# Kernel optimization log

Hardware: AMD Instinct MI355X
Metric: run time of the kernel (lower is better)

## Reference

```python
import jax, jax.numpy as jnp
import numpy as np

N = 100000   # nodes
E = 1600000  # edges
F_IN = 64    # n_features
H = 32       # hidden_size
OUT = 1      # output_size


def _lin(k, fan_in, fan_out):
    return (jax.random.normal(k, (fan_in, fan_out), jnp.float32) / np.sqrt(fan_in)).astype(jnp.float32)


def setup_inputs() -> dict:
    key = jax.random.key(0)
    ks = jax.random.split(key, 16)
    x = jax.random.normal(ks[0], (N, F_IN), jnp.float32)
    edge_index = jax.random.randint(ks[1], (2, E), 0, N, dtype=jnp.int64)
    # guarantee current_node (=0) has outgoing edges so the legal-move mask is non-empty
    edge_index = edge_index.at[0, :64].set(0)
    edge_attr = jax.random.uniform(ks[2], (E,), jnp.float32)
    return {
        "x": x, "edge_index": edge_index, "edge_attr": edge_attr, "current_node": 0,
        # conv_in: GraphConv(F_IN -> H)
        "Win_rel": _lin(ks[3], F_IN, H), "bin_rel": jnp.zeros((H,), jnp.float32), "Win_root": _lin(ks[4], F_IN, H),
        # conv_hidden: GraphConv(H -> H)
        "Wh_rel": _lin(ks[5], H, H), "bh_rel": jnp.zeros((H,), jnp.float32), "Wh_root": _lin(ks[6], H, H),
        # policy_conv: GraphConv(H -> OUT)
        "Wp_rel": _lin(ks[7], H, OUT), "bp_rel": jnp.zeros((OUT,), jnp.float32), "Wp_root": _lin(ks[8], H, OUT),
        # value_conv: GraphConv(H -> OUT)
        "Wv_rel": _lin(ks[9], H, OUT), "bv_rel": jnp.zeros((OUT,), jnp.float32), "Wv_root": _lin(ks[10], H, OUT),
    }


def _graph_conv(h, src, dst, ew, W_rel, b_rel, W_root):
    # PyG GraphConv: out_i = W_root h_i + W_rel * sum_{j->i} e_ji * h_j + b
    msg = h[src] * ew[:, None]                              # [E, d] gather + scale
    agg = jax.ops.segment_sum(msg, dst, num_segments=N)      # [N, d] scatter-add
    return agg @ W_rel + b_rel + h @ W_root


def reference(x, edge_index, edge_attr, current_node,
              Win_rel, bin_rel, Win_root,
              Wh_rel, bh_rel, Wh_root,
              Wp_rel, bp_rel, Wp_root,
              Wv_rel, bv_rel, Wv_root):
    src, dst = edge_index[0], edge_index[1]
    h = jax.nn.relu(_graph_conv(x, src, dst, edge_attr, Win_rel, bin_rel, Win_root))
    h = jax.nn.relu(_graph_conv(h, src, dst, edge_attr, Wh_rel, bh_rel, Wh_root))
    p = _graph_conv(h, src, dst, edge_attr, Wp_rel, bp_rel, Wp_root)  # [N, 1]
    v = _graph_conv(h, src, dst, edge_attr, Wv_rel, bv_rel, Wv_root)  # [N, 1]
    # illegal_moves_mask: 1 for nodes directly reachable from current_node
    hit = (src == current_node).astype(jnp.float32)
    mask = (jnp.zeros((N,), jnp.float32).at[dst].add(hit) > 0).astype(jnp.float32)
    p_m = mask * p.T                                   # [1, N]
    p_m = jnp.where(p_m == 0, -jnp.inf, p_m)
    p_soft = jax.nn.softmax(p_m, axis=1)
    v_m = mask * v.T                                   # [1, N]
    return p_soft.reshape(-1), v_m.reshape(-1)
```

## Files before the change

### kernel.cpp

```cpp
#include <hip/hip_runtime.h>
#include <hip/hip_fp16.h>
#include <cmath>

static constexpr int NN = 100000;
static constexpr int NE = 1600000;
static const size_t NW = (size_t)NN * 32;
static constexpr int SUB = 256;
static constexpr int NSUB = 391;
static constexpr int CH = 8192;
static constexpr int NCH = (NE + CH - 1) / CH;
static constexpr int BCAP = 5200;
static constexpr int CSRN = NSUB * BCAP;
static constexpr int MCAP = 4096;

__device__ __forceinline__ float ent_w(unsigned e)
{
    return __half2float(__ushort_as_half((unsigned short)(e >> 17)));
}
__device__ __forceinline__ int ent_s(unsigned e)
{
    int s = (int)(e & 0x1FFFF);
    return s < NN ? s : NN - 1;
}

__device__ __forceinline__ float4 pack8(const float* v)
{
    union { __half2 h2[4]; float4 f4; } u;
    u.h2[0] = __floats2half2_rn(v[0], v[1]);
    u.h2[1] = __floats2half2_rn(v[2], v[3]);
    u.h2[2] = __floats2half2_rn(v[4], v[5]);
    u.h2[3] = __floats2half2_rn(v[6], v[7]);
    return u.f4;
}

__global__ void __launch_bounds__(512) fused_build_mm1_k(
    const int* __restrict__ src, const int* __restrict__ dst,
    const float* __restrict__ ew, const int* __restrict__ curp,
    int* __restrict__ maskb, int* __restrict__ mcount, int* __restrict__ mlist,
    int* __restrict__ bcnt, unsigned* __restrict__ bx,
    unsigned char* __restrict__ bd,
    const float* __restrict__ x, const float* __restrict__ Wrel,
    const float* __restrict__ Wroot, const float* __restrict__ bin,
    __half* __restrict__ proj1, __half* __restrict__ root1)
{
    __shared__ union {
        struct {
            unsigned sBufX[CH];
            unsigned char sBufD[CH];
            int lhist[NSUB];
            int lpos[NSUB];
            int lstart[NSUB];
            int lbase[NSUB];
            int tscan[512];
        } s;
        struct {
            float sX[128 * 65];
            float sW[64 * 68];
        } m;
    } u;

    int t = threadIdx.x;
    int bid = blockIdx.x;

    if (bid < NCH) {
        for (int i = t; i < NSUB; i += 512) { u.s.lhist[i] = 0; u.s.lpos[i] = 0; }
        __syncthreads();
        int c0 = bid * CH;
        int cur = curp[0];
        unsigned rx[CH / 512];
        int rd[CH / 512];
#pragma unroll
        for (int it = 0; it < CH / 512; ++it) {
            int e = c0 + it * 512 + t;
            rd[it] = -1;
            if (e < NE) {
                int d = dst[e];
                int sv = src[e];
                if ((unsigned)d < (unsigned)NN) {
                    rd[it] = d;
                    unsigned bits = __half_as_ushort(__float2half(ew[e]));
                    rx[it] = ((unsigned)sv & 0x1FFFF) | (bits << 17);
                    atomicAdd(&u.s.lhist[d >> 8], 1);
                    if (sv == cur) {
                        if (atomicExch(maskb + d, 1) == 0) {
                            int idx = atomicAdd(mcount, 1);
                            if (idx < MCAP) mlist[idx] = d;
                        }
                    }
                }
            }
        }
        __syncthreads();
        int v = (t < NSUB) ? u.s.lhist[t] : 0;
        u.s.tscan[t] = v;
        __syncthreads();
        for (int sh = 1; sh < 512; sh <<= 1) {
            int xv = u.s.tscan[t];
            int a = (t >= sh) ? u.s.tscan[t - sh] : 0;
            __syncthreads();
            u.s.tscan[t] = xv + a;
            __syncthreads();
        }
        if (t < NSUB) {
            u.s.lstart[t] = u.s.tscan[t] - v;
            u.s.lbase[t] = (v > 0) ? atomicAdd(&bcnt[t], v) : 0;
        }
        __syncthreads();
#pragma unroll
        for (int it = 0; it < CH / 512; ++it) {
            if (rd[it] >= 0) {
                int b = rd[it] >> 8;
                int p = atomicAdd(&u.s.lpos[b], 1);
                int pos = u.s.lstart[b] + p;
                u.s.sBufX[pos] = rx[it];
                u.s.sBufD[pos] = (unsigned char)(rd[it] & 255);
            }
        }
        __syncthreads();
        int grp = t >> 4, l16 = t & 15;
        for (int b = grp; b < NSUB; b += 32) {
            int s0 = u.s.lstart[b];
            int cb = u.s.lhist[b];
            int gb = u.s.lbase[b];
            size_t gb0 = (size_t)b * BCAP;
            for (int j = l16; j < cb; j += 16) {
                unsigned pos = (unsigned)(gb + j);
                if (pos < (unsigned)BCAP) {
                    bx[gb0 + pos] = u.s.sBufX[s0 + j];
                    bd[gb0 + pos] = u.s.sBufD[s0 + j];
                }
            }
        }
    } else {
        int mb = bid - NCH;
        for (int i = t; i < 64 * 32; i += 512) {
            int k = i >> 5, j = i & 31;
            u.m.sW[k * 68 + j] = Wrel[i];
            u.m.sW[k * 68 + 32 + j] = Wroot[i];
        }
        int base = mb * 128;
        for (int i = t; i < 2048; i += 512) {
            int node = i >> 4;
            int k = (i & 15) * 4;
            int n = base + node;
            if (n >= NN) n = NN - 1;
            float4 v4 = *(const float4*)(x + (size_t)n * 64 + k);
            float* p = u.m.sX + node * 65 + k;
            p[0] = v4.x; p[1] = v4.y; p[2] = v4.z; p[3] = v4.w;
        }
        __syncthreads();
        int cg = t & 7;
        int ng = t >> 3;
        int c0m = 8 * cg;
        float acc[2][8] = {};
        for (int k = 0; k < 64; ++k) {
            float xv0 = u.m.sX[(2 * ng + 0) * 65 + k];
            float xv1 = u.m.sX[(2 * ng + 1) * 65 + k];
            float4 w0 = *(const float4*)(u.m.sW + k * 68 + c0m);
            float4 w1 = *(const float4*)(u.m.sW + k * 68 + c0m + 4);
            const float* wp = (const float*)&w0;
#pragma unroll
            for (int j = 0; j < 4; ++j) {
                float w = wp[j];
                acc[0][j] = fmaf(xv0, w, acc[0][j]);
                acc[1][j] = fmaf(xv1, w, acc[1][j]);
            }
            const float* wq = (const float*)&w1;
#pragma unroll
            for (int j = 0; j < 4; ++j) {
                float w = wq[j];
                acc[0][4 + j] = fmaf(xv0, w, acc[0][4 + j]);
                acc[1][4 + j] = fmaf(xv1, w, acc[1][4 + j]);
            }
        }
#pragma unroll
        for (int r = 0; r < 2; ++r) {
            int n = base + 2 * ng + r;
            if (n >= NN) break;
            if (cg < 4) {
                *(float4*)(proj1 + (size_t)n * 32 + c0m) = pack8(acc[r]);
            } else {
                int c = c0m - 32;
                float vv[8];
#pragma unroll
                for (int j = 0; j < 8; ++j) vv[j] = acc[r][j] + bin[c + j];
                *(float4*)(root1 + (size_t)n * 32 + c) = pack8(vv);
            }
        }
    }
}

__global__ void __launch_bounds__(1024) sortagg1_k(
    const unsigned* __restrict__ bx, const unsigned char* __restrict__ bd,
    const int* __restrict__ bcnt,
    const __half* __restrict__ proj1, const __half* __restrict__ root1,
    unsigned* __restrict__ csr4, int* __restrict__ deg, int* __restrict__ off,
    __half* __restrict__ h1)
{
    __shared__ unsigned sX[BCAP];
    __shared__ unsigned char sD[BCAP];
    __shared__ unsigned sE[BCAP];
    __shared__ int lhist[SUB];
    __shared__ int lstart[SUB];
    __shared__ int lcur[SUB];
    __shared__ int tscan[256];
    int g = blockIdx.x, t = threadIdx.x;
    if (t < SUB) { lhist[t] = 0; lcur[t] = 0; }
    __syncthreads();
    int cnt = bcnt[g];
    if (cnt < 0) cnt = 0;
    if (cnt > BCAP) cnt = BCAP;
    size_t gbase = (size_t)g * BCAP;
    for (int i = t; i < cnt; i += 1024) {
        unsigned e = bx[gbase + i];
        unsigned char d = bd[gbase + i];
        sX[i] = e;
        sD[i] = d;
        atomicAdd(&lhist[d], 1);
    }
    __syncthreads();
    if (t < 256) tscan[t] = lhist[t];
    __syncthreads();
    for (int s = 1; s < 256; s <<= 1) {
        int x = 0, a = 0;
        if (t < 256) { x = tscan[t]; a = (t >= s) ? tscan[t - s] : 0; }
        __syncthreads();
        if (t < 256) tscan[t] = x + a;
        __syncthreads();
    }
    if (t < 256) lstart[t] = tscan[t] - lhist[t];
    __syncthreads();
    for (int i = t; i < cnt; i += 1024) {
        int ld = (int)sD[i];
        int p = atomicAdd(&lcur[ld], 1);
        int pos = lstart[ld] + p;
        if ((unsigned)pos < (unsigned)BCAP) sE[pos] = sX[i];
    }
    __syncthreads();
    int base = g * BCAP;
    if (t < SUB) {
        int n = g * SUB + t;
        if (n < NN) {
            deg[n] = lhist[t];
            off[n] = base + lstart[t];
        }
    }
    for (int i = t; i < cnt; i += 1024) {
        unsigned pos = (unsigned)(base + i);
        if (pos < (unsigned)CSRN) csr4[pos] = sE[i];
    }
    int q = t & 3;
    int f0 = q * 8;
    int l = t >> 2;
    int n = g * SUB + l;
    if (n >= NN) return;
    int st = lstart[l];
    int dg = lhist[l];
    if (st < 0) st = 0;
    if (st > BCAP) st = BCAP;
    if (dg < 0) dg = 0;
    if (dg > BCAP - st) dg = BCAP - st;
    float acc[8] = {0.f, 0.f, 0.f, 0.f, 0.f, 0.f, 0.f, 0.f};
    int i = 0;
    for (; i + 1 < dg; i += 2) {
        unsigned e0 = sE[st + i];
        unsigned e1 = sE[st + i + 1];
        float w0 = ent_w(e0), w1 = ent_w(e1);
        float4 r0 = *(const float4*)(proj1 + (size_t)ent_s(e0) * 32 + f0);
        float4 r1 = *(const float4*)(proj1 + (size_t)ent_s(e1) * 32 + f0);
        const __half2* h0 = (const __half2*)&r0;
        const __half2* h1p = (const __half2*)&r1;
#pragma unroll
        for (int u = 0; u < 4; ++u) {
            float2 a = __half22float2(h0[u]);
            float2 b = __half22float2(h1p[u]);
            acc[2 * u] = fmaf(w0, a.x, acc[2 * u]);
            acc[2 * u + 1] = fmaf(w0, a.y, acc[2 * u + 1]);
            acc[2 * u] = fmaf(w1, b.x, acc[2 * u]);
            acc[2 * u + 1] = fmaf(w1, b.y, acc[2 * u + 1]);
        }
    }
    if (i < dg) {
        unsigned e0 = sE[st + i];
        float w0 = ent_w(e0);
        float4 r0 = *(const float4*)(proj1 + (size_t)ent_s(e0) * 32 + f0);
        const __half2* h0 = (const __half2*)&r0;
#pragma unroll
        for (int u = 0; u < 4; ++u) {
            float2 a = __half22float2(h0[u]);
            acc[2 * u] = fmaf(w0, a.x, acc[2 * u]);
            acc[2 * u + 1] = fmaf(w0, a.y, acc[2 * u + 1]);
        }
    }
    float4 rr = *(const float4*)(root1 + (size_t)n * 32 + f0);
    const __half2* rp = (const __half2*)&rr;
    float h[8];
#pragma unroll
    for (int u = 0; u < 4; ++u) {
        float2 f2 = __half22float2(rp[u]);
        h[2 * u] = fmaxf(acc[2 * u] + f2.x, 0.f);
        h[2 * u + 1] = fmaxf(acc[2 * u + 1] + f2.y, 0.f);
    }
    *(float4*)(h1 + (size_t)n * 32 + f0) = pack8(h);
}

__global__ void __launch_bounds__(256) mm2_k(
    const __half* __restrict__ h1, const float* __restrict__ Wrel,
    const float* __restrict__ Wroot, const float* __restrict__ bh,
    __half* __restrict__ proj2, __half* __restrict__ root2)
{
    __shared__ float sX[128 * 33];
    __shared__ float sW[32 * 68];
    int t = threadIdx.x;
    for (int i = t; i < 32 * 32; i += 256) {
        int k = i >> 5, j = i & 31;
        sW[k * 68 + j] = Wrel[i];
        sW[k * 68 + 32 + j] = Wroot[i];
    }
    int base = blockIdx.x * 128;
    for (int i = t; i < 512; i += 256) {
        int node = i >> 2;
        int hs = (i & 3) * 8;
        int n = base + node;
        if (n >= NN) n = NN - 1;
        float4 v = *(const float4*)(h1 + (size_t)n * 32 + hs);
        const __half2* hp = (const __half2*)&v;
        float* p = sX + node * 33 + hs;
#pragma unroll
        for (int u = 0; u < 4; ++u) {
            float2 f2 = __half22float2(hp[u]);
            p[2 * u] = f2.x;
            p[2 * u + 1] = f2.y;
        }
    }
    __syncthreads();
    int cg = t & 7;
    int ng = t >> 3;
    int c0 = 8 * cg;
    float acc[4][8] = {};
    for (int k = 0; k < 32; ++k) {
        float xv0 = sX[(4 * ng + 0) * 33 + k];
        float xv1 = sX[(4 * ng + 1) * 33 + k];
        float xv2 = sX[(4 * ng + 2) * 33 + k];
        float xv3 = sX[(4 * ng + 3) * 33 + k];
        float4 w0 = *(const float4*)(sW + k * 68 + c0);
        float4 w1 = *(const float4*)(sW + k * 68 + c0 + 4);
        const float* wp = (const float*)&w0;
#pragma unroll
        for (int j = 0; j < 4; ++j) {
            float w = wp[j];
            acc[0][j] = fmaf(xv0, w, acc[0][j]);
            acc[1][j] = fmaf(xv1, w, acc[1][j]);
            acc[2][j] = fmaf(xv2, w, acc[2][j]);
            acc[3][j] = fmaf(xv3, w, acc[3][j]);
        }
        const float* wq = (const float*)&w1;
#pragma unroll
        for (int j = 0; j < 4; ++j) {
            float w = wq[j];
            acc[0][4 + j] = fmaf(xv0, w, acc[0][4 + j]);
            acc[1][4 + j] = fmaf(xv1, w, acc[1][4 + j]);
            acc[2][4 + j] = fmaf(xv2, w, acc[2][4 + j]);
            acc[3][4 + j] = fmaf(xv3, w, acc[3][4 + j]);
        }
    }
#pragma unroll
    for (int r = 0; r < 4; ++r) {
        int n = base + 4 * ng + r;
        if (n >= NN) break;
        if (cg < 4) {
            *(float4*)(proj2 + (size_t)n * 32 + c0) = pack8(acc[r]);
        } else {
            int c = c0 - 32;
            float v[8];
#pragma unroll
            for (int j = 0; j < 8; ++j) v[j] = acc[r][j] + bh[c + j];
            *(float4*)(root2 + (size_t)n * 32 + c) = pack8(v);
        }
    }
}

__global__ void __launch_bounds__(256) agg2_v4(
    const __half* __restrict__ proj2, const __half* __restrict__ root2,
    const float* __restrict__ Wp_rel, const float* __restrict__ Wp_root,
    const float* __restrict__ bp, const float* __restrict__ Wv_rel,
    const float* __restrict__ Wv_root, const float* __restrict__ bv,
    const unsigned* __restrict__ csr4, const int* __restrict__ off,
    const int* __restrict__ deg, float2* __restrict__ pv,
    float* __restrict__ pbase, float* __restrict__ vbase,
    float* __restrict__ out_p, float* __restrict__ out_v)
{
    __shared__ float sHead[4 * 32];
    if (threadIdx.x < 32) {
        sHead[threadIdx.x] = Wp_rel[threadIdx.x];
        sHead[32 + threadIdx.x] = Wp_root[threadIdx.x];
        sHead[64 + threadIdx.x] = Wv_rel[threadIdx.x];
        sHead[96 + threadIdx.x] = Wv_root[threadIdx.x];
    }
    __syncthreads();
    int t = threadIdx.x;
    int q = t & 3;
    int f0 = q * 8;
    int n = blockIdx.x * 64 + (t >> 2);
    if (n >= NN) return;
    int st = off[n];
    int dg = deg[n];
    if (st < 0) st = 0;
    if (st > CSRN) st = CSRN;
    if (dg < 0) dg = 0;
    if (dg > CSRN - st) dg = CSRN - st;
    float acc[8] = {0.f, 0.f, 0.f, 0.f, 0.f, 0.f, 0.f, 0.f};
    int i = 0;
    for (; i + 1 < dg; i += 2) {
        unsigned e0 = csr4[st + i];
        unsigned e1 = csr4[st + i + 1];
        float w0 = ent_w(e0), w1 = ent_w(e1);
        float4 r0 = *(const float4*)(proj2 + (size_t)ent_s(e0) * 32 + f0);
        float4 r1 = *(const float4*)(proj2 + (size_t)ent_s(e1) * 32 + f0);
        const __half2* h0 = (const __half2*)&r0;
        const __half2* h1p = (const __half2*)&r1;
#pragma unroll
        for (int u = 0; u < 4; ++u) {
            float2 a = __half22float2(h0[u]);
            float2 b = __half22float2(h1p[u]);
            acc[2 * u] = fmaf(w0, a.x, acc[2 * u]);
            acc[2 * u + 1] = fmaf(w0, a.y, acc[2 * u + 1]);
            acc[2 * u] = fmaf(w1, b.x, acc[2 * u]);
            acc[2 * u + 1] = fmaf(w1, b.y, acc[2 * u + 1]);
        }
    }
    if (i < dg) {
        unsigned e0 = csr4[st + i];
        float w0 = ent_w(e0);
        float4 r0 = *(const float4*)(proj2 + (size_t)ent_s(e0) * 32 + f0);
        const __half2* h0 = (const __half2*)&r0;
#pragma unroll
        for (int u = 0; u < 4; ++u) {
            float2 a = __half22float2(h0[u]);
            acc[2 * u] = fmaf(w0, a.x, acc[2 * u]);
            acc[2 * u + 1] = fmaf(w0, a.y, acc[2 * u + 1]);
        }
    }
    float4 rr = *(const float4*)(root2 + (size_t)n * 32 + f0);
    const __half2* rp = (const __half2*)&rr;
    float h[8];
#pragma unroll
    for (int u = 0; u < 4; ++u) {
        float2 f2 = __half22float2(rp[u]);
        h[2 * u] = fmaxf(acc[2 * u] + f2.x, 0.f);
        h[2 * u + 1] = fmaxf(acc[2 * u + 1] + f2.y, 0.f);
    }
    float prv = 0.f, pov = 0.f, vrv = 0.f, vov = 0.f;
#pragma unroll
    for (int j = 0; j < 8; ++j) {
        prv = fmaf(h[j], sHead[f0 + j], prv);
        pov = fmaf(h[j], sHead[32 + f0 + j], pov);
        vrv = fmaf(h[j], sHead[64 + f0 + j], vrv);
        vov = fmaf(h[j], sHead[96 + f0 + j], vov);
    }
#pragma unroll
    for (int m = 1; m <= 2; m <<= 1) {
        prv += __shfl_xor(prv, m, 64);
        pov += __shfl_xor(pov, m, 64);
        vrv += __shfl_xor(vrv, m, 64);
        vov += __shfl_xor(vov, m, 64);
    }
    if (q == 0) {
        pv[n] = make_float2(prv, vrv);
        pbase[n] = pov + bp[0];
        vbase[n] = vov + bv[0];
        out_p[n] = 0.f;
        out_v[n] = 0.f;
    }
}

__global__ void __launch_bounds__(256) masked_softmax_k(
    const int* __restrict__ mlist, const int* __restrict__ mcount,
    const unsigned* __restrict__ csr4, const int* __restrict__ off,
    const int* __restrict__ deg, const float2* __restrict__ pv,
    const float* __restrict__ pbase, const float* __restrict__ vbase,
    float* __restrict__ out_p, float* __restrict__ out_v)
{
    __shared__ float sPm[MCAP];
    __shared__ float sV[MCAP];
    __shared__ int sN[MCAP];
    __shared__ float sMx, sSum;
    __shared__ float sred[4];
    int m = mcount[0];
    if (m > MCAP) m = MCAP;
    if (m < 0) m = 0;
    for (int idx = threadIdx.x; idx < m; idx += 256) {
        int n = mlist[idx];
        if ((unsigned)n >= (unsigned)NN) n = 0;
        sN[idx] = n;
        int st = off[n];
        int dg = deg[n];
        if (st < 0) st = 0;
        if (st > CSRN) st = CSRN;
        if (dg < 0) dg = 0;
        if (dg > CSRN - st) dg = CSRN - st;
        float pa = 0.f, va = 0.f;
        for (int i = 0; i < dg; ++i) {
            unsigned ent = csr4[st + i];
            int s = ent_s(ent);
            float w = ent_w(ent);
            float2 tv = pv[s];
            pa = fmaf(tv.x, w, pa);
            va = fmaf(tv.y, w, va);
        }
        float p = pa + pbase[n];
        sPm[idx] = (p == 0.f) ? -INFINITY : p;
        sV[idx] = va + vbase[n];
    }
    __syncthreads();
    float mx = -INFINITY;
    for (int i = threadIdx.x; i < m; i += 256) mx = fmaxf(mx, sPm[i]);
#pragma unroll
    for (int k = 32; k; k >>= 1) mx = fmaxf(mx, __shfl_xor(mx, k, 64));
    if ((threadIdx.x & 63) == 0) sred[threadIdx.x >> 6] = mx;
    __syncthreads();
    if (threadIdx.x == 0)
        sMx = fmaxf(fmaxf(sred[0], sred[1]), fmaxf(sred[2], sred[3]));
    __syncthreads();
    float sum = 0.f;
    for (int i = threadIdx.x; i < m; i += 256) {
        float x = sPm[i];
        sum += (x == -INFINITY) ? 0.f : expf(x - sMx);
    }
#pragma unroll
    for (int k = 32; k; k >>= 1) sum += __shfl_xor(sum, k, 64);
    if ((threadIdx.x & 63) == 0) sred[threadIdx.x >> 6] = sum;
    __syncthreads();
    if (threadIdx.x == 0) sSum = sred[0] + sred[1] + sred[2] + sred[3];
    __syncthreads();
    for (int idx = threadIdx.x; idx < m; idx += 256) {
        int n = sN[idx];
        float x = sPm[idx];
        out_p[n] = (x == -INFINITY) ? 0.f : expf(x - sMx) / sSum;
        out_v[n] = sV[idx];
    }
}

extern "C" void kernel_launch(void* const* d_in, const int* in_sizes, int n_in,
                              void* d_out, int out_size, void* d_ws,
                              size_t ws_size, hipStream_t stream)
{
    const float* x        = (const float*)d_in[0];
    const int*   ei       = (const int*)d_in[1];
    const float* ew       = (const float*)d_in[2];
    const int*   cur      = (const int*)d_in[3];
    const float* Win_rel  = (const float*)d_in[4];
    const float* bin_rel  = (const float*)d_in[5];
    const float* Win_root = (const float*)d_in[6];
    const float* Wh_rel   = (const float*)d_in[7];
    const float* bh_rel   = (const float*)d_in[8];
    const float* Wh_root  = (const float*)d_in[9];
    const float* Wp_rel   = (const float*)d_in[10];
    const float* bp       = (const float*)d_in[11];
    const float* Wp_root  = (const float*)d_in[12];
    const float* Wv_rel   = (const float*)d_in[13];
    const float* bv       = (const float*)d_in[14];
    const float* Wv_root  = (const float*)d_in[15];

    const int* srcA = ei;
    const int* dstA = ei + NE;

    char* w8 = (char*)d_ws;
    unsigned* csr4 = (unsigned*)w8;
    int* deg    = (int*)(csr4 + CSRN);
    int* off    = deg + NN;
    int* maskb  = off + NN;
    int* mcount = maskb + NN;
    int* bcnt   = mcount + 8;
    int* mlist  = bcnt + 400;
    __half* proj1 = (__half*)(mlist + MCAP);
    __half* root1 = proj1 + NW;
    __half* h1    = root1 + NW;
    __half* proj2 = h1 + NW;
    __half* root2 = proj2 + NW;
    float2* pv    = (float2*)(root2 + NW);
    float* pbase  = (float*)(pv + NN);
    float* vbase  = pbase + NN;
    unsigned* bucket_x = (unsigned*)(vbase + NN);
    unsigned char* bucket_d = (unsigned char*)(bucket_x + CSRN);

    float* out_p = (float*)d_out;
    float* out_v = out_p + NN;

    const int NB_MM    = (NN + 127) / 128;
    const int NB_AGG   = (NN + 63) / 64;
    const int NB_FUSED = NCH + NB_MM;

    hipMemsetAsync(maskb, 0, ((size_t)NN + 8 + 400) * sizeof(int), stream);

    fused_build_mm1_k<<<NB_FUSED, 512, 0, stream>>>(
        srcA, dstA, ew, cur, maskb, mcount, mlist, bcnt, bucket_x, bucket_d,
        x, Win_rel, Win_root, bin_rel, proj1, root1);
    sortagg1_k<<<NSUB, 1024, 0, stream>>>(bucket_x, bucket_d, bcnt,
                                          proj1, root1, csr4, deg, off, h1);
    mm2_k<<<NB_MM, 256, 0, stream>>>(h1, Wh_rel, Wh_root, bh_rel, proj2, root2);
    agg2_v4<<<NB_AGG, 256, 0, stream>>>(proj2, root2, Wp_rel, Wp_root, bp,
                                        Wv_rel, Wv_root, bv, csr4, off, deg,
                                        pv, pbase, vbase, out_p, out_v);
    masked_softmax_k<<<1, 256, 0, stream>>>(mlist, mcount, csr4, off, deg, pv,
                                            pbase, vbase, out_p, out_v);
}
```

Before: 229.1 us.

## Fuse layer-1 aggregation with layer-2 projection matmul in one kernel

```diff
diff --git a/kernel.cpp b/kernel.cpp
--- a/kernel.cpp
+++ b/kernel.cpp
@@ -190,21 +190,32 @@
     }
 }
 
-__global__ void __launch_bounds__(1024) sortagg1_k(
+__global__ void __launch_bounds__(1024) sortagg1mm2_k(
     const unsigned* __restrict__ bx, const unsigned char* __restrict__ bd,
     const int* __restrict__ bcnt,
     const __half* __restrict__ proj1, const __half* __restrict__ root1,
+    const float* __restrict__ Wrel, const float* __restrict__ Wroot,
+    const float* __restrict__ bh,
     unsigned* __restrict__ csr4, int* __restrict__ deg, int* __restrict__ off,
-    __half* __restrict__ h1)
-{
-    __shared__ unsigned sX[BCAP];
-    __shared__ unsigned char sD[BCAP];
-    __shared__ unsigned sE[BCAP];
-    __shared__ int lhist[SUB];
-    __shared__ int lstart[SUB];
-    __shared__ int lcur[SUB];
-    __shared__ int tscan[256];
+    __half* __restrict__ proj2, __half* __restrict__ root2)
+{
+    __shared__ __align__(16) char smem[59600];
+    unsigned* sX = (unsigned*)(smem);
+    unsigned char* sD = (unsigned char*)(smem + 20800);
+    unsigned* sE = (unsigned*)(smem + 26000);
+    int* lhist  = (int*)(smem + 46800);
+    int* lstart = (int*)(smem + 47824);
+    int* lcur   = (int*)(smem + 48848);
+    int* tscan  = (int*)(smem + 49872);
+    float* sW   = (float*)(smem + 50896);
+    float* sH   = (float*)(smem);
+
     int g = blockIdx.x, t = threadIdx.x;
+    {
+        int k = t >> 5, j = t & 31;
+        sW[k * 68 + j] = Wrel[t];
+        sW[k * 68 + 32 + j] = Wroot[t];
+    }
     if (t < SUB) { lhist[t] = 0; lcur[t] = 0; }
     __syncthreads();
     int cnt = bcnt[g];
@@ -253,129 +264,97 @@
     int f0 = q * 8;
     int l = t >> 2;
     int n = g * SUB + l;
-    if (n >= NN) return;
-    int st = lstart[l];
-    int dg = lhist[l];
-    if (st < 0) st = 0;
-    if (st > BCAP) st = BCAP;
-    if (dg < 0) dg = 0;
-    if (dg > BCAP - st) dg = BCAP - st;
-    float acc[8] = {0.f, 0.f, 0.f, 0.f, 0.f, 0.f, 0.f, 0.f};
-    int i = 0;
-    for (; i + 1 < dg; i += 2) {
-        unsigned e0 = sE[st + i];
-        unsigned e1 = sE[st + i + 1];
-        float w0 = ent_w(e0), w1 = ent_w(e1);
-        float4 r0 = *(const float4*)(proj1 + (size_t)ent_s(e0) * 32 + f0);
-        float4 r1 = *(const float4*)(proj1 + (size_t)ent_s(e1) * 32 + f0);
-        const __half2* h0 = (const __half2*)&r0;
-        const __half2* h1p = (const __half2*)&r1;
+    bool act = (n < NN);
+    float h[8] = {};
+    if (act) {
+        int st = lstart[l];
+        int dg = lhist[l];
+        if (st < 0) st = 0;
+        if (st > BCAP) st = BCAP;
+        if (dg < 0) dg = 0;
+        if (dg > BCAP - st) dg = BCAP - st;
+        float acc[8] = {0.f, 0.f, 0.f, 0.f, 0.f, 0.f, 0.f, 0.f};
+        int i = 0;
+        for (; i + 1 < dg; i += 2) {
+            unsigned e0 = sE[st + i];
+            unsigned e1 = sE[st + i + 1];
+            float w0 = ent_w(e0), w1 = ent_w(e1);
+            float4 r0 = *(const float4*)(proj1 + (size_t)ent_s(e0) * 32 + f0);
+            float4 r1 = *(const float4*)(proj1 + (size_t)ent_s(e1) * 32 + f0);
+            const __half2* h0 = (const __half2*)&r0;
+            const __half2* h1p = (const __half2*)&r1;
+#pragma unroll
+            for (int u = 0; u < 4; ++u) {
+                float2 a = __half22float2(h0[u]);
+                float2 b = __half22float2(h1p[u]);
+                acc[2 * u] = fmaf(w0, a.x, acc[2 * u]);
+                acc[2 * u + 1] = fmaf(w0, a.y, acc[2 * u + 1]);
+                acc[2 * u] = fmaf(w1, b.x, acc[2 * u]);
+                acc[2 * u + 1] = fmaf(w1, b.y, acc[2 * u + 1]);
+            }
+        }
+        if (i < dg) {
+            unsigned e0 = sE[st + i];
+            float w0 = ent_w(e0);
+            float4 r0 = *(const float4*)(proj1 + (size_t)ent_s(e0) * 32 + f0);
+            const __half2* h0 = (const __half2*)&r0;
+#pragma unroll
+            for (int u = 0; u < 4; ++u) {
+                float2 a = __half22float2(h0[u]);
+                acc[2 * u] = fmaf(w0, a.x, acc[2 * u]);
+                acc[2 * u + 1] = fmaf(w0, a.y, acc[2 * u + 1]);
+            }
+        }
+        float4 rr = *(const float4*)(root1 + (size_t)n * 32 + f0);
+        const __half2* rp = (const __half2*)&rr;
 #pragma unroll
         for (int u = 0; u < 4; ++u) {
-            float2 a = __half22float2(h0[u]);
-            float2 b = __half22float2(h1p[u]);
-            acc[2 * u] = fmaf(w0, a.x, acc[2 * u]);
-            acc[2 * u + 1] = fmaf(w0, a.y, acc[2 * u + 1]);
-            acc[2 * u] = fmaf(w1, b.x, acc[2 * u]);
-            acc[2 * u + 1] = fmaf(w1, b.y, acc[2 * u + 1]);
-        }
-    }
-    if (i < dg) {
-        unsigned e0 = sE[st + i];
-        float w0 = ent_w(e0);
-        float4 r0 = *(const float4*)(proj1 + (size_t)ent_s(e0) * 32 + f0);
-        const __half2* h0 = (const __half2*)&r0;
-#pragma unroll
-        for (int u = 0; u < 4; ++u) {
-            float2 a = __half22float2(h0[u]);
-            acc[2 * u] = fmaf(w0, a.x, acc[2 * u]);
-            acc[2 * u + 1] = fmaf(w0, a.y, acc[2 * u + 1]);
-        }
-    }
-    float4 rr = *(const float4*)(root1 + (size_t)n * 32 + f0);
-    const __half2* rp = (const __half2*)&rr;
-    float h[8];
-#pragma unroll
-    for (int u = 0; u < 4; ++u) {
-        float2 f2 = __half22float2(rp[u]);
-        h[2 * u] = fmaxf(acc[2 * u] + f2.x, 0.f);
-        h[2 * u + 1] = fmaxf(acc[2 * u + 1] + f2.y, 0.f);
-    }
-    *(float4*)(h1 + (size_t)n * 32 + f0) = pack8(h);
-}
-
-__global__ void __launch_bounds__(256) mm2_k(
-    const __half* __restrict__ h1, const float* __restrict__ Wrel,
-    const float* __restrict__ Wroot, const float* __restrict__ bh,
-    __half* __restrict__ proj2, __half* __restrict__ root2)
-{
-    __shared__ float sX[128 * 33];
-    __shared__ float sW[32 * 68];
-    int t = threadIdx.x;
-    for (int i = t; i < 32 * 32; i += 256) {
-        int k = i >> 5, j = i & 31;
-        sW[k * 68 + j] = Wrel[i];
-        sW[k * 68 + 32 + j] = Wroot[i];
-    }
-    int base = blockIdx.x * 128;
-    for (int i = t; i < 512; i += 256) {
-        int node = i >> 2;
-        int hs = (i & 3) * 8;
-        int n = base + node;
-        if (n >= NN) n = NN - 1;
-        float4 v = *(const float4*)(h1 + (size_t)n * 32 + hs);
-        const __half2* hp = (const __half2*)&v;
-        float* p = sX + node * 33 + hs;
-#pragma unroll
-        for (int u = 0; u < 4; ++u) {
-            float2 f2 = __half22float2(hp[u]);
-            p[2 * u] = f2.x;
-            p[2 * u + 1] = f2.y;
-        }
-    }
-    __syncthreads();
-    int cg = t & 7;
-    int ng = t >> 3;
-    int c0 = 8 * cg;
-    float acc[4][8] = {};
+            float2 f2 = __half22float2(rp[u]);
+            h[2 * u] = fmaxf(acc[2 * u] + f2.x, 0.f);
+            h[2 * u + 1] = fmaxf(acc[2 * u + 1] + f2.y, 0.f);
+        }
+#pragma unroll
+        for (int j = 0; j < 8; ++j)
+            h[j] = __half2float(__float2half_rn(h[j]));
+    }
+    __syncthreads();
+#pragma unroll
+    for (int j = 0; j < 8; ++j) sH[l * 33 + f0 + j] = h[j];
+    __syncthreads();
+    int cg = t & 7, ng = t >> 3, c0 = 8 * cg;
+    float a2[2][8] = {};
     for (int k = 0; k < 32; ++k) {
-        float xv0 = sX[(4 * ng + 0) * 33 + k];
-        float xv1 = sX[(4 * ng + 1) * 33 + k];
-        float xv2 = sX[(4 * ng + 2) * 33 + k];
-        float xv3 = sX[(4 * ng + 3) * 33 + k];
+        float x0 = sH[(2 * ng + 0) * 33 + k];
+        float x1 = sH[(2 * ng + 1) * 33 + k];
         float4 w0 = *(const float4*)(sW + k * 68 + c0);
         float4 w1 = *(const float4*)(sW + k * 68 + c0 + 4);
         const float* wp = (const float*)&w0;
 #pragma unroll
         for (int j = 0; j < 4; ++j) {
             float w = wp[j];
-            acc[0][j] = fmaf(xv0, w, acc[0][j]);
-            acc[1][j] = fmaf(xv1, w, acc[1][j]);
-            acc[2][j] = fmaf(xv2, w, acc[2][j]);
-            acc[3][j] = fmaf(xv3, w, acc[3][j]);
+            a2[0][j] = fmaf(x0, w, a2[0][j]);
+            a2[1][j] = fmaf(x1, w, a2[1][j]);
         }
         const float* wq = (const float*)&w1;
 #pragma unroll
         for (int j = 0; j < 4; ++j) {
             float w = wq[j];
-            acc[0][4 + j] = fmaf(xv0, w, acc[0][4 + j]);
-            acc[1][4 + j] = fmaf(xv1, w, acc[1][4 + j]);
-            acc[2][4 + j] = fmaf(xv2, w, acc[2][4 + j]);
-            acc[3][4 + j] = fmaf(xv3, w, acc[3][4 + j]);
-        }
-    }
-#pragma unroll
-    for (int r = 0; r < 4; ++r) {
-        int n = base + 4 * ng + r;
-        if (n >= NN) break;
+            a2[0][4 + j] = fmaf(x0, w, a2[0][4 + j]);
+            a2[1][4 + j] = fmaf(x1, w, a2[1][4 + j]);
+        }
+    }
+#pragma unroll
+    for (int r = 0; r < 2; ++r) {
+        int n2 = g * SUB + 2 * ng + r;
+        if (n2 >= NN) break;
         if (cg < 4) {
-            *(float4*)(proj2 + (size_t)n * 32 + c0) = pack8(acc[r]);
+            *(float4*)(proj2 + (size_t)n2 * 32 + c0) = pack8(a2[r]);
         } else {
             int c = c0 - 32;
-            float v[8];
-#pragma unroll
-            for (int j = 0; j < 8; ++j) v[j] = acc[r][j] + bh[c + j];
-            *(float4*)(root2 + (size_t)n * 32 + c) = pack8(v);
+            float vv[8];
+#pragma unroll
+            for (int j = 0; j < 8; ++j) vv[j] = a2[r][j] + bh[c + j];
+            *(float4*)(root2 + (size_t)n2 * 32 + c) = pack8(vv);
         }
     }
 }
@@ -575,8 +554,7 @@
     int* mlist  = bcnt + 400;
     __half* proj1 = (__half*)(mlist + MCAP);
     __half* root1 = proj1 + NW;
-    __half* h1    = root1 + NW;
-    __half* proj2 = h1 + NW;
+    __half* proj2 = root1 + NW;
     __half* root2 = proj2 + NW;
     float2* pv    = (float2*)(root2 + NW);
     float* pbase  = (float*)(pv + NN);
@@ -596,9 +574,10 @@
     fused_build_mm1_k<<<NB_FUSED, 512, 0, stream>>>(
         srcA, dstA, ew, cur, maskb, mcount, mlist, bcnt, bucket_x, bucket_d,
         x, Win_rel, Win_root, bin_rel, proj1, root1);
-    sortagg1_k<<<NSUB, 1024, 0, stream>>>(bucket_x, bucket_d, bcnt,
-                                          proj1, root1, csr4, deg, off, h1);
-    mm2_k<<<NB_MM, 256, 0, stream>>>(h1, Wh_rel, Wh_root, bh_rel, proj2, root2);
+    sortagg1mm2_k<<<NSUB, 1024, 0, stream>>>(bucket_x, bucket_d, bcnt,
+                                             proj1, root1,
+                                             Wh_rel, Wh_root, bh_rel,
+                                             csr4, deg, off, proj2, root2);
     agg2_v4<<<NB_AGG, 256, 0, stream>>>(proj2, root2, Wp_rel, Wp_root, bp,
                                         Wv_rel, Wv_root, bv, csr4, off, deg,
                                         pv, pbase, vbase, out_p, out_v);
```

After: 362.5 us. 58.2% more time.
